# Performance work log

Measured on AMD Instinct MI355X. Metric: run time of the kernel, lower is better.

The kernel has to match this reference:

```python
import jax, jax.numpy as jnp
import numpy as np
import math

B, CK, T, H, W = 4, 64, 8, 30, 54
N, CV = 8, 512

def setup_inputs() -> dict:
    key = jax.random.key(0)
    k1, k2, k3, k4 = jax.random.split(key, 4)
    mem_keys = jax.random.normal(k1, (B, CK, T, H, W), dtype=jnp.float32)
    mem_values = jax.random.normal(k2, (N, CV, T, H, W), dtype=jnp.float32)
    qk = jax.random.normal(k3, (B, CK, H, W), dtype=jnp.float32)
    broadcast_map = jax.random.randint(k4, (N,), 0, B, dtype=jnp.int64)
    return {"mem_keys": mem_keys, "mem_values": mem_values, "qk": qk,
            "broadcast_map": broadcast_map}

def reference(mem_keys, mem_values, qk, broadcast_map):
    # STCNModel.read_memory
    Bq, CKq, Tq, Hq, Wq = mem_keys.shape
    mk = mem_keys.reshape(Bq, CKq, Tq * Hq * Wq)      # [B, CK, THW]
    q = qk.reshape(Bq, CKq, Hq * Wq)                   # [B, CK, HW]
    a_sq = jnp.sum(mk * mk, axis=1)[:, :, None]        # [B, THW, 1]
    ab = jnp.einsum('bct,bcq->btq', mk, q)             # [B, THW, HW]
    frame_affinity = (2.0 * ab - a_sq) / math.sqrt(CKq)
    # softmax over memory dim (axis=1)
    frame_affinity = jax.nn.softmax(frame_affinity, axis=1)
    obj_affinity = frame_affinity[broadcast_map]       # [N, THW, HW]
    Nn, CVv = mem_values.shape[0], mem_values.shape[1]
    mo = mem_values.reshape(Nn, CVv, Tq * Hq * Wq)     # [N, CV, THW]
    obj_read = jnp.einsum('nct,ntq->ncq', mo, obj_affinity)
    return obj_read.reshape(Nn, CVv, Hq, Wq)
```

## Files before the change

kernel.cpp:

```cpp
#include <hip/hip_runtime.h>
#include <hip/hip_bf16.h>

#define CKDIM 64
#define THW   12960
#define HWDIM 1620
#define NOBJ  8
#define CVAL  512
#define NB    4
#define NSTEP 405
#define NJT   13
#define NCHS  8
#define NCHP  4
#define PCH   16
#define S2F   0.3606737602222409f

#if defined(__has_builtin)
#if __has_builtin(__builtin_amdgcn_global_load_lds)
#define HAVE_GLL 1
#endif
#endif

using bf16x8 = __attribute__((ext_vector_type(8))) short;
using f32x4  = __attribute__((ext_vector_type(4))) float;

__device__ __forceinline__ unsigned cvtpk(float lo, float hi) {
    unsigned r;
    asm("v_cvt_pk_bf16_f32 %0, %1, %2" : "=v"(r) : "v"(lo), "v"(hi));
    return r;
}
__device__ __forceinline__ unsigned short bf_rne(float x) {
    unsigned u = __float_as_uint(x);
    u += 0x7FFFu + ((u >> 16) & 1u);
    return (unsigned short)(u >> 16);
}
__device__ __forceinline__ float fexp2(float x) {
#if __has_builtin(__builtin_amdgcn_exp2f)
    return __builtin_amdgcn_exp2f(x);
#else
    return __expf(x * 0.69314718055994531f);
#endif
}
#ifdef HAVE_GLL
__device__ __forceinline__ void gload16(const void* g, void* l) {
    __builtin_amdgcn_global_load_lds(
        (const __attribute__((address_space(1))) unsigned int*)g,
        (__attribute__((address_space(3))) unsigned int*)l, 16, 0, 0);
}
#endif

__global__ void stcn_ksq_kernel(const float* __restrict__ mk, float* __restrict__ k8l) {
    int t = blockIdx.x * 256 + threadIdx.x;
    if (t >= THW) return;
    int b = blockIdx.y;
    const float* p = mk + (size_t)b * CKDIM * THW + t;
    float s = 0.f;
#pragma unroll
    for (int c = 0; c < CKDIM; ++c) { float v = p[(size_t)c * THW]; s = fmaf(v, v, s); }
    k8l[b * THW + t] = s * (0.125f * 1.44269504088896341f);
}

__global__ __launch_bounds__(512)
void stcn_ktr_kernel(const float* __restrict__ mk, unsigned short* __restrict__ kbt,
                     float* __restrict__ k8l) {
    __shared__ unsigned short L[64][72];
    __shared__ float S[64][8];
    const int tid = threadIdx.x, b = blockIdx.y, t0 = blockIdx.x * 64;
    const int tt = tid & 63;
    float a2 = 0.f;
#pragma unroll
    for (int it = 0; it < 8; ++it) {
        int idx = tid + 512 * it;
        int c = idx >> 6;
        int t = t0 + tt;
        float v = (t < THW) ? mk[((size_t)b * CKDIM + c) * THW + t] : 0.f;
        L[tt][c] = bf_rne(v);
        a2 = fmaf(v, v, a2);
    }
    S[tt][tid >> 6] = a2;
    __syncthreads();
    if (tid < 64) {
        float s = 0.f;
#pragma unroll
        for (int q = 0; q < 8; ++q) s += S[tid][q];
        int t = t0 + tid;
        if (t < THW) k8l[b * THW + t] = s * (0.125f * 1.44269504088896341f);
    }
    {
        int tr = tid >> 3, cq = tid & 7;
        int t = t0 + tr;
        if (t < THW) {
            uint4 o = *(const uint4*)&L[tr][8 * cq];
            *(uint4*)(kbt + ((size_t)b * THW + t) * CKDIM + 8 * cq) = o;
        }
    }
}

__global__ void stcn_vcvt_kernel(const float* __restrict__ mv, unsigned short* __restrict__ mvb) {
    size_t i = ((size_t)blockIdx.x * 256 + threadIdx.x) * 8;
    if (i >= (size_t)NOBJ * CVAL * THW) return;
    float4 v0 = *(const float4*)(mv + i);
    float4 v1 = *(const float4*)(mv + i + 4);
    uint4 o;
    o.x = cvtpk(v0.x, v0.y); o.y = cvtpk(v0.z, v0.w);
    o.z = cvtpk(v1.x, v1.y); o.w = cvtpk(v1.z, v1.w);
    *(uint4*)(mvb + i) = o;
}

template <int MODE, bool VB16, bool KB16>
__global__ __launch_bounds__(512, (MODE == 1) ? 4 : 1)
void stcn_aff_kernel(const float* __restrict__ mk, const unsigned short* __restrict__ kbt,
                     const float* __restrict__ qk, const float* __restrict__ k8l,
                     float* __restrict__ mpart, float* __restrict__ lpart,
                     const float* __restrict__ mv, const unsigned short* __restrict__ mvb,
                     const int* __restrict__ bmap, float* __restrict__ out)
{
    constexpr int SMEM_BYTES = (MODE == 0) ? 36864 : 45312;
    __shared__ __align__(16) unsigned char smem[SMEM_BYTES];
    unsigned short* KtP   = (unsigned short*)smem;
    float*          k8tP  = (float*)(smem + 9216);
    unsigned short* PtP   = (unsigned short*)(smem + 9472);
    unsigned short* VtP   = (unsigned short*)(smem + 23808);
    float*          mjsP  = (float*)(smem + 44288);
    float*          iljsP = (float*)(smem + 44800);
    unsigned short* QtP   = (unsigned short*)smem;

    const int tid  = threadIdx.x;
    const int w    = tid >> 6;
    const int lane = tid & 63;
    const int g    = lane >> 4;
    const int lr   = lane & 15;

    int b, n = 0, jt, kc, cb = 0;
    if (MODE == 0) { b = blockIdx.y; jt = blockIdx.x >> 3; kc = blockIdx.x & 7; }
    else {
        n = blockIdx.y; jt = blockIdx.x >> 3; kc = (blockIdx.x >> 1) & 3; cb = blockIdx.x & 1;
        b = bmap[n];
    }
    const int jbase = jt * 128;
    const int cbase = cb * 256;

#pragma unroll
    for (int it = 0; it < 8; ++it) {
        int idx = tid + 512 * it;
        int j = idx & 127, cp = idx >> 7;
        int jg = jbase + j;
        float q0 = 0.f, q1 = 0.f;
        if (jg < HWDIM) {
            const float* qp = qk + ((size_t)b * CKDIM + 2 * cp) * HWDIM + jg;
            q0 = qp[0]; q1 = qp[HWDIM];
        }
        unsigned wh = cvtpk(q0, q1);
        float r0 = q0 - __uint_as_float(wh << 16);
        float r1 = q1 - __uint_as_float(wh & 0xFFFF0000u);
        *(unsigned*)&QtP[(0 * 128 + j) * 72 + 2 * cp] = wh;
        *(unsigned*)&QtP[(1 * 128 + j) * 72 + 2 * cp] = cvtpk(r0, r1);
    }
    __syncthreads();
    bf16x8 bqh[2], bql[2];
#pragma unroll
    for (int s = 0; s < 2; ++s) {
        bqh[s] = *(const bf16x8*)&QtP[(0 * 128 + w * 16 + lr) * 72 + 32 * s + 8 * g];
        bql[s] = *(const bf16x8*)&QtP[(1 * 128 + w * 16 + lr) * 72 + 32 * s + 8 * g];
    }
    __syncthreads();

    auto stageK_loads = [&](int st, uint2& k16, float2* kvf) {
        if constexpr (KB16) {
            int tt = tid >> 4, cq = tid & 15;
            k16 = *(const uint2*)(kbt + ((size_t)b * THW + st * 32 + tt) * CKDIM + 4 * cq);
        } else {
#pragma unroll
            for (int it = 0; it < 2; ++it) {
                int idx = tid + 512 * it;
                int tt = idx & 31, cp = idx >> 5;
                const float* kp = mk + ((size_t)b * CKDIM + 2 * cp) * THW + st * 32 + tt;
                kvf[it].x = kp[0];
                kvf[it].y = kp[THW];
            }
        }
    };
    auto stageK_write = [&](int buf, uint2 k16, const float2* kvf) {
        if constexpr (KB16) {
            int tt = tid >> 4, cq = tid & 15;
            *(uint2*)&KtP[(buf * 32 + tt) * 72 + 4 * cq] = k16;
        } else {
#pragma unroll
            for (int it = 0; it < 2; ++it) {
                int idx = tid + 512 * it;
                int tt = idx & 31, cp = idx >> 5;
                *(unsigned*)&KtP[(buf * 32 + tt) * 72 + 2 * cp] = cvtpk(kvf[it].x, kvf[it].y);
            }
        }
    };

    int s0, s1;
    if (MODE == 0) { s0 = (NSTEP * kc) / NCHS; s1 = (NSTEP * (kc + 1)) / NCHS; }
    else           { s0 = (NSTEP * kc) / NCHP; s1 = (NSTEP * (kc + 1)) / NCHP; }

    if (MODE == 1 && tid < 128) {
        int jg = jbase + tid;
        float m = 0.f, l = 0.f;
        if (jg < HWDIM) {
            m = -1e30f;
#pragma unroll
            for (int c = 0; c < NCHS; ++c) {
                float mc = mpart[(b * NCHS + c) * HWDIM + jg];
                float lc = lpart[(b * NCHS + c) * HWDIM + jg];
                float mn = fmaxf(m, mc);
                l = l * fexp2(m - mn) + lc * fexp2(mc - mn);
                m = mn;
            }
        }
        mjsP[tid]  = m;
        iljsP[tid] = (l > 0.f) ? 1.f / l : 0.f;
    }
    {
        uint2 k16; float2 kvf[2];
        stageK_loads(s0, k16, kvf);
        stageK_write(0, k16, kvf);
        if (tid < 32) k8tP[tid] = k8l[b * THW + s0 * 32 + tid];
    }
    __syncthreads();

    float mv_j = 0.f, il_j = 0.f;
    if (MODE == 1) { mv_j = mjsP[w * 16 + lr]; il_j = iljsP[w * 16 + lr]; }

    float m_run = -1e30f, l_run = 0.f;
    f32x4 zz = {0.f, 0.f, 0.f, 0.f};
    f32x4 acc[4][4];
    if (MODE == 1)
#pragma unroll
        for (int i = 0; i < 4; ++i)
#pragma unroll
            for (int j = 0; j < 4; ++j) acc[i][j] = zz;

    const int wc = w >> 1, wj = w & 1;
    const int vc = tid >> 1, vth = tid & 1;

    int cur = 0;
    for (int st = s0; st < s1; ++st) {
        const int t0 = st * 32;
        const bool nxt = (st + 1 < s1);

        uint4 vw0 = {0,0,0,0}, vw1 = {0,0,0,0};
        if (MODE == 1) {
            if (VB16) {
                const unsigned short* vp = mvb + ((size_t)n * CVAL + cbase + vc) * THW + t0 + vth * 16;
                vw0 = *(const uint4*)vp;
                vw1 = *(const uint4*)(vp + 8);
            } else {
                const float* vp = mv + ((size_t)n * CVAL + cbase + vc) * THW + t0 + vth * 16;
                float4 f0 = *(const float4*)vp;
                float4 f1 = *(const float4*)(vp + 4);
                float4 f2 = *(const float4*)(vp + 8);
                float4 f3 = *(const float4*)(vp + 12);
                vw0 = make_uint4(cvtpk(f0.x,f0.y), cvtpk(f0.z,f0.w), cvtpk(f1.x,f1.y), cvtpk(f1.z,f1.w));
                vw1 = make_uint4(cvtpk(f2.x,f2.y), cvtpk(f2.z,f2.w), cvtpk(f3.x,f3.y), cvtpk(f3.z,f3.w));
            }
        }
        uint2 k16; float2 kvf[2];
        float k8next = 0.f;
        if (nxt) {
            stageK_loads(st + 1, k16, kvf);
            if (tid < 32) k8next = k8l[b * THW + (st + 1) * 32 + tid];
        }
        bf16x8 ak0[2], ak1[2];
#pragma unroll
        for (int s = 0; s < 2; ++s) {
            ak0[s] = *(const bf16x8*)&KtP[(cur * 32 + lr) * 72 + 32 * s + 8 * g];
            ak1[s] = *(const bf16x8*)&KtP[(cur * 32 + 16 + lr) * 72 + 32 * s + 8 * g];
        }
        f32x4 k80 = *(const f32x4*)&k8tP[cur * 32 + 4 * g];
        f32x4 k81 = *(const f32x4*)&k8tP[cur * 32 + 16 + 4 * g];
        f32x4 ab0 = zz, ab1 = zz;
#pragma unroll
        for (int s = 0; s < 2; ++s) {
            ab0 = __builtin_amdgcn_mfma_f32_16x16x32_bf16(ak0[s], bqh[s], ab0, 0, 0, 0);
            ab0 = __builtin_amdgcn_mfma_f32_16x16x32_bf16(ak0[s], bql[s], ab0, 0, 0, 0);
            ab1 = __builtin_amdgcn_mfma_f32_16x16x32_bf16(ak1[s], bqh[s], ab1, 0, 0, 0);
            ab1 = __builtin_amdgcn_mfma_f32_16x16x32_bf16(ak1[s], bql[s], ab1, 0, 0, 0);
        }
        if (nxt) {
            stageK_write(cur ^ 1, k16, kvf);
            if (tid < 32) k8tP[(cur ^ 1) * 32 + tid] = k8next;
        }

        if (MODE == 0) {
            float L0[4], L1[4], tmax = -1e30f;
#pragma unroll
            for (int r = 0; r < 4; ++r) {
                L0[r] = fmaf(ab0[r], S2F, -k80[r]); tmax = fmaxf(tmax, L0[r]);
                L1[r] = fmaf(ab1[r], S2F, -k81[r]); tmax = fmaxf(tmax, L1[r]);
            }
            float ps = 0.f;
#pragma unroll
            for (int r = 0; r < 4; ++r)
                ps += fexp2(L0[r] - tmax) + fexp2(L1[r] - tmax);
            float mn = fmaxf(m_run, tmax);
            l_run = l_run * fexp2(m_run - mn) + ps * fexp2(tmax - mn);
            m_run = mn;
            __syncthreads();
        } else {
            float p0[4], p1[4];
#pragma unroll
            for (int r = 0; r < 4; ++r) {
                p0[r] = fexp2(fmaf(ab0[r], S2F, -k80[r]) - mv_j) * il_j;
                p1[r] = fexp2(fmaf(ab1[r], S2F, -k81[r]) - mv_j) * il_j;
            }
            __syncthreads();
            {
                int jl = w * 16 + lr;
                *(uint2*)&PtP[jl * 56 + 4 * g]      = make_uint2(cvtpk(p0[0], p0[1]), cvtpk(p0[2], p0[3]));
                *(uint2*)&PtP[jl * 56 + 16 + 4 * g] = make_uint2(cvtpk(p1[0], p1[1]), cvtpk(p1[2], p1[3]));
                *(uint4*)&VtP[vc * 40 + vth * 16]     = vw0;
                *(uint4*)&VtP[vc * 40 + vth * 16 + 8] = vw1;
            }
            __syncthreads();
            bf16x8 bp[4];
#pragma unroll
            for (int jf = 0; jf < 4; ++jf)
                bp[jf] = *(const bf16x8*)&PtP[(wj * 64 + jf * 16 + lr) * 56 + 8 * g];
#pragma unroll
            for (int cf = 0; cf < 4; ++cf) {
                bf16x8 av = *(const bf16x8*)&VtP[(wc * 64 + cf * 16 + lr) * 40 + 8 * g];
#pragma unroll
                for (int jf = 0; jf < 4; ++jf)
                    acc[cf][jf] = __builtin_amdgcn_mfma_f32_16x16x32_bf16(av, bp[jf], acc[cf][jf], 0, 0, 0);
            }
        }
        cur ^= 1;
    }

    if (MODE == 0) {
#pragma unroll
        for (int off = 16; off < 64; off <<= 1) {
            float mo = __shfl_xor(m_run, off, 64);
            float lo = __shfl_xor(l_run, off, 64);
            float mn = fmaxf(m_run, mo);
            l_run = l_run * fexp2(m_run - mn) + lo * fexp2(mo - mn);
            m_run = mn;
        }
        int jg = jbase + w * 16 + lr;
        if (g == 0 && jg < HWDIM) {
            mpart[(b * NCHS + kc) * HWDIM + jg] = m_run;
            lpart[(b * NCHS + kc) * HWDIM + jg] = l_run;
        }
    } else {
#pragma unroll
        for (int cf = 0; cf < 4; ++cf) {
#pragma unroll
            for (int jf = 0; jf < 4; ++jf) {
                int jg = jbase + wj * 64 + jf * 16 + lr;
                if (jg < HWDIM) {
                    int c = cbase + wc * 64 + cf * 16 + 4 * g;
                    float* op = out + ((size_t)n * CVAL + c) * HWDIM + jg;
#pragma unroll
                    for (int r = 0; r < 4; ++r)
                        atomicAdd(op + (size_t)r * HWDIM, acc[cf][jf][r]);
                }
            }
        }
    }
}

__global__ __launch_bounds__(512)
void stcn_pwrite_kernel(const unsigned short* __restrict__ kbt,
                        const float* __restrict__ qk, const float* __restrict__ k8l,
                        const float* __restrict__ mpart, const float* __restrict__ lpart,
                        unsigned short* __restrict__ Pws, int bbase)
{
    __shared__ __align__(16) unsigned char smem[36864];
    unsigned short* KtP   = (unsigned short*)smem;
    float*          k8tP  = (float*)(smem + 9216);
    unsigned short* PtP   = (unsigned short*)(smem + 9472);
    float*          mjsP  = (float*)(smem + 23808);
    float*          iljsP = (float*)(smem + 24320);
    unsigned short* QtP   = (unsigned short*)smem;

    const int tid  = threadIdx.x;
    const int w    = tid >> 6;
    const int lane = tid & 63;
    const int g    = lane >> 4;
    const int lr   = lane & 15;

    const int bb = blockIdx.y;
    const int b  = bbase + bb;
    const int jt = blockIdx.x >> 4, kc = blockIdx.x & 15;
    const int jbase = jt * 128;

#pragma unroll
    for (int it = 0; it < 8; ++it) {
        int idx = tid + 512 * it;
        int j = idx & 127, cp = idx >> 7;
        int jg = jbase + j;
        float q0 = 0.f, q1 = 0.f;
        if (jg < HWDIM) {
            const float* qp = qk + ((size_t)b * CKDIM + 2 * cp) * HWDIM + jg;
            q0 = qp[0]; q1 = qp[HWDIM];
        }
        unsigned wh = cvtpk(q0, q1);
        float r0 = q0 - __uint_as_float(wh << 16);
        float r1 = q1 - __uint_as_float(wh & 0xFFFF0000u);
        *(unsigned*)&QtP[(0 * 128 + j) * 72 + 2 * cp] = wh;
        *(unsigned*)&QtP[(1 * 128 + j) * 72 + 2 * cp] = cvtpk(r0, r1);
    }
    __syncthreads();
    bf16x8 bqh[2], bql[2];
#pragma unroll
    for (int s = 0; s < 2; ++s) {
        bqh[s] = *(const bf16x8*)&QtP[(0 * 128 + w * 16 + lr) * 72 + 32 * s + 8 * g];
        bql[s] = *(const bf16x8*)&QtP[(1 * 128 + w * 16 + lr) * 72 + 32 * s + 8 * g];
    }
    __syncthreads();

    const int s0 = (NSTEP * kc) / PCH, s1 = (NSTEP * (kc + 1)) / PCH;

    if (tid < 128) {
        int jg = jbase + tid;
        float m = 0.f, l = 0.f;
        if (jg < HWDIM) {
            m = -1e30f;
#pragma unroll
            for (int c = 0; c < NCHS; ++c) {
                float mc = mpart[(b * NCHS + c) * HWDIM + jg];
                float lc = lpart[(b * NCHS + c) * HWDIM + jg];
                float mn = fmaxf(m, mc);
                l = l * fexp2(m - mn) + lc * fexp2(mc - mn);
                m = mn;
            }
        }
        mjsP[tid]  = m;
        iljsP[tid] = (l > 0.f) ? 1.f / l : 0.f;
    }
    {
        int tt = tid >> 4, cq = tid & 15;
        uint2 k16 = *(const uint2*)(kbt + ((size_t)b * THW + s0 * 32 + tt) * CKDIM + 4 * cq);
        *(uint2*)&KtP[tt * 72 + 4 * cq] = k16;
        if (tid < 32) k8tP[tid] = k8l[b * THW + s0 * 32 + tid];
    }
    __syncthreads();

    const float mv_j = mjsP[w * 16 + lr], il_j = iljsP[w * 16 + lr];
    f32x4 zz = {0.f, 0.f, 0.f, 0.f};

    int cur = 0;
    for (int st = s0; st < s1; ++st) {
        const int t0 = st * 32;
        const bool nxt = (st + 1 < s1);
        uint2 k16;
        float k8next = 0.f;
        const int tt = tid >> 4, cq = tid & 15;
        if (nxt) {
            k16 = *(const uint2*)(kbt + ((size_t)b * THW + (st + 1) * 32 + tt) * CKDIM + 4 * cq);
            if (tid < 32) k8next = k8l[b * THW + (st + 1) * 32 + tid];
        }
        bf16x8 ak0[2], ak1[2];
#pragma unroll
        for (int s = 0; s < 2; ++s) {
            ak0[s] = *(const bf16x8*)&KtP[(cur * 32 + lr) * 72 + 32 * s + 8 * g];
            ak1[s] = *(const bf16x8*)&KtP[(cur * 32 + 16 + lr) * 72 + 32 * s + 8 * g];
        }
        f32x4 k80 = *(const f32x4*)&k8tP[cur * 32 + 4 * g];
        f32x4 k81 = *(const f32x4*)&k8tP[cur * 32 + 16 + 4 * g];
        f32x4 ab0 = zz, ab1 = zz;
#pragma unroll
        for (int s = 0; s < 2; ++s) {
            ab0 = __builtin_amdgcn_mfma_f32_16x16x32_bf16(ak0[s], bqh[s], ab0, 0, 0, 0);
            ab0 = __builtin_amdgcn_mfma_f32_16x16x32_bf16(ak0[s], bql[s], ab0, 0, 0, 0);
            ab1 = __builtin_amdgcn_mfma_f32_16x16x32_bf16(ak1[s], bqh[s], ab1, 0, 0, 0);
            ab1 = __builtin_amdgcn_mfma_f32_16x16x32_bf16(ak1[s], bql[s], ab1, 0, 0, 0);
        }
        if (nxt) {
            *(uint2*)&KtP[((cur ^ 1) * 32 + tt) * 72 + 4 * cq] = k16;
            if (tid < 32) k8tP[(cur ^ 1) * 32 + tid] = k8next;
        }
        float p0[4], p1[4];
#pragma unroll
        for (int r = 0; r < 4; ++r) {
            p0[r] = fexp2(fmaf(ab0[r], S2F, -k80[r]) - mv_j) * il_j;
            p1[r] = fexp2(fmaf(ab1[r], S2F, -k81[r]) - mv_j) * il_j;
        }
        __syncthreads();
        {
            int jl = w * 16 + lr;
            *(uint2*)&PtP[jl * 56 + 4 * g]      = make_uint2(cvtpk(p0[0], p0[1]), cvtpk(p0[2], p0[3]));
            *(uint2*)&PtP[jl * 56 + 16 + 4 * g] = make_uint2(cvtpk(p1[0], p1[1]), cvtpk(p1[2], p1[3]));
        }
        __syncthreads();
        {
            int jr = tid >> 2, qq = tid & 3;
            int jg = jbase + jr;
            if (jg < HWDIM)
                *(uint4*)(Pws + ((size_t)bb * HWDIM + jg) * THW + t0 + qq * 8) =
                    *(const uint4*)&PtP[jr * 56 + qq * 8];
        }
        cur ^= 1;
    }
}

template <bool FULLP>
__global__ __launch_bounds__(256, 4)
void stcn_gemm3_kernel(const unsigned short* __restrict__ mvb,
                       const unsigned short* __restrict__ Pws,
                       const int* __restrict__ bmap, float* __restrict__ out, int phase)
{
    __shared__ __align__(16) unsigned short Av[2][128 * 32];
    __shared__ __align__(16) unsigned short Bv[2][128 * 32];

    int n, cm, jn, ks, ksplit;
    if constexpr (FULLP) {
        int wg  = blockIdx.x;
        int vid = (wg & 7) * 208 + (wg >> 3);
        n = vid / 208;
        int r  = vid % 208;
        cm = r / 52;
        int r2 = r % 52;
        jn = r2 >> 2;
        ks = r2 & 3;
        ksplit = 4;
    } else {
        n = blockIdx.y;
        const int x = blockIdx.x;
        ks = x & 1;
        const int rest = x >> 1;
        jn = rest % NJT;
        cm = rest / NJT;
        ksplit = 2;
    }
    const int b = bmap[n];
    int bslot;
    if constexpr (FULLP) { bslot = b; }
    else { if ((b >> 1) != phase) return; bslot = b & 1; }

    const int jbase = jn * 128, cbase = cm * 128;

    const int tid = threadIdx.x;
    const int w = tid >> 6, lane = tid & 63, g = lane >> 4, lr = lane & 15;
    const int wc = w >> 1, wj = w & 1;

    const int srow = tid >> 2;
    const int tsw  = (((tid & 3) ^ ((tid >> 3) & 3)) << 3);
    const int gs8  = ((g ^ ((lr >> 1) & 3)) << 3);

    const int s0 = (NSTEP * ks) / ksplit, s1 = (NSTEP * (ks + 1)) / ksplit;

    const unsigned short* abase = mvb + ((size_t)n * CVAL + cbase) * THW;
    const unsigned short* bbase = Pws + (size_t)bslot * HWDIM * THW;
    int jr0 = jbase + srow;       if (jr0 >= HWDIM) jr0 = 0;
    int jr1 = jbase + 64 + srow;  if (jr1 >= HWDIM) jr1 = 0;
    const unsigned short* ga0 = abase + (size_t)(srow) * THW + tsw;
    const unsigned short* ga1 = abase + (size_t)(64 + srow) * THW + tsw;
    const unsigned short* gb0 = bbase + (size_t)jr0 * THW + tsw;
    const unsigned short* gb1 = bbase + (size_t)jr1 * THW + tsw;

    f32x4 zz = {0.f, 0.f, 0.f, 0.f};
    f32x4 acc[4][4];
#pragma unroll
    for (int i = 0; i < 4; ++i)
#pragma unroll
        for (int j = 0; j < 4; ++j) acc[i][j] = zz;

#ifdef HAVE_GLL
    auto stage = [&](int buf, int st) {
        const int t0 = st * 32;
        gload16(ga0 + t0, &Av[buf][0    + w * 512]);
        gload16(ga1 + t0, &Av[buf][2048 + w * 512]);
        gload16(gb0 + t0, &Bv[buf][0    + w * 512]);
        gload16(gb1 + t0, &Bv[buf][2048 + w * 512]);
    };
    stage(0, s0);
#else
    {
        const int t0 = s0 * 32;
        *(uint4*)&Av[0][tid * 8]        = *(const uint4*)(ga0 + t0);
        *(uint4*)&Av[0][2048 + tid * 8] = *(const uint4*)(ga1 + t0);
        *(uint4*)&Bv[0][tid * 8]        = *(const uint4*)(gb0 + t0);
        *(uint4*)&Bv[0][2048 + tid * 8] = *(const uint4*)(gb1 + t0);
    }
#endif
    __syncthreads();

    int cur = 0;
    for (int st = s0; st < s1; ++st) {
        const bool nxt = (st + 1 < s1);
#ifdef HAVE_GLL
        if (nxt) stage(cur ^ 1, st + 1);
#else
        uint4 ra0, ra1, rb0, rb1;
        if (nxt) {
            const int t0 = (st + 1) * 32;
            ra0 = *(const uint4*)(ga0 + t0);
            ra1 = *(const uint4*)(ga1 + t0);
            rb0 = *(const uint4*)(gb0 + t0);
            rb1 = *(const uint4*)(gb1 + t0);
        }
#endif
        bf16x8 av[4], bp[4];
#pragma unroll
        for (int cf = 0; cf < 4; ++cf)
            av[cf] = *(const bf16x8*)&Av[cur][(wc * 64 + cf * 16 + lr) * 32 + gs8];
#pragma unroll
        for (int jf = 0; jf < 4; ++jf)
            bp[jf] = *(const bf16x8*)&Bv[cur][(wj * 64 + jf * 16 + lr) * 32 + gs8];
#pragma unroll
        for (int cf = 0; cf < 4; ++cf)
#pragma unroll
            for (int jf = 0; jf < 4; ++jf)
                acc[cf][jf] = __builtin_amdgcn_mfma_f32_16x16x32_bf16(av[cf], bp[jf], acc[cf][jf], 0, 0, 0);
#ifndef HAVE_GLL
        if (nxt) {
            *(uint4*)&Av[cur ^ 1][tid * 8]        = ra0;
            *(uint4*)&Av[cur ^ 1][2048 + tid * 8] = ra1;
            *(uint4*)&Bv[cur ^ 1][tid * 8]        = rb0;
            *(uint4*)&Bv[cur ^ 1][2048 + tid * 8] = rb1;
        }
#endif
        __syncthreads();
        cur ^= 1;
    }

#pragma unroll
    for (int cf = 0; cf < 4; ++cf)
#pragma unroll
        for (int jf = 0; jf < 4; ++jf) {
            int jg = jbase + wj * 64 + jf * 16 + lr;
            if (jg < HWDIM) {
                int c = cbase + wc * 64 + cf * 16 + 4 * g;
                float* op = out + ((size_t)n * CVAL + c) * HWDIM + jg;
#pragma unroll
                for (int r = 0; r < 4; ++r)
                    atomicAdd(op + (size_t)r * HWDIM, acc[cf][jf][r]);
            }
        }
}

extern "C" void kernel_launch(void* const* d_in, const int* in_sizes, int n_in,
                              void* d_out, int out_size, void* d_ws, size_t ws_size,
                              hipStream_t stream) {
    (void)in_sizes; (void)n_in;
    const float* mk   = (const float*)d_in[0];
    const float* mv   = (const float*)d_in[1];
    const float* qkp  = (const float*)d_in[2];
    const int*   bmap = (const int*)d_in[3];
    float* out = (float*)d_out;

    float* k8l   = (float*)d_ws;
    float* mpart = k8l + NB * THW;
    float* lpart = mpart + NB * NCHS * HWDIM;
    unsigned short* mvb = (unsigned short*)(lpart + NB * NCHS * HWDIM);
    unsigned short* kbt = mvb + (size_t)NOBJ * CVAL * THW;
    unsigned short* Pws = kbt + (size_t)NB * THW * CKDIM;

    size_t base_bytes = (size_t)(NB * THW + 2 * NB * NCHS * HWDIM) * 4;
    size_t need_vb  = base_bytes + (size_t)NOBJ * CVAL * THW * 2;
    size_t need_kbt = need_vb + (size_t)NB * THW * CKDIM * 2;
    size_t need_P2  = need_kbt + (size_t)2 * HWDIM * THW * 2;
    size_t need_P4  = need_kbt + (size_t)4 * HWDIM * THW * 2;
    bool use_vb16 = (ws_size >= need_vb);
    bool use_kbt  = (ws_size >= need_kbt);
    bool use_P2   = (ws_size >= need_P2);
    bool use_P4   = (ws_size >= need_P4);

    hipMemsetAsync(d_out, 0, (size_t)out_size * sizeof(float), stream);
    if (use_kbt)
        stcn_ktr_kernel<<<dim3((THW + 63) / 64, NB), 512, 0, stream>>>(mk, kbt, k8l);
    else
        stcn_ksq_kernel<<<dim3((THW + 255) / 256, NB), 256, 0, stream>>>(mk, k8l);
    if (use_vb16) {
        size_t nthreads = (size_t)NOBJ * CVAL * THW / 8;
        stcn_vcvt_kernel<<<(unsigned)((nthreads + 255) / 256), 256, 0, stream>>>(mv, mvb);
    }

    if (use_kbt)
        stcn_aff_kernel<0, false, true><<<dim3(NJT * NCHS, NB), 512, 0, stream>>>(
            mk, kbt, qkp, k8l, mpart, lpart, nullptr, nullptr, nullptr, nullptr);
    else
        stcn_aff_kernel<0, false, false><<<dim3(NJT * NCHS, NB), 512, 0, stream>>>(
            mk, nullptr, qkp, k8l, mpart, lpart, nullptr, nullptr, nullptr, nullptr);

    if (use_P4 && use_kbt) {
        stcn_pwrite_kernel<<<dim3(NJT * PCH, NB), 512, 0, stream>>>(
            kbt, qkp, k8l, mpart, lpart, Pws, 0);
        stcn_gemm3_kernel<true><<<dim3(1664), 256, 0, stream>>>(
            mvb, Pws, bmap, out, 0);
    } else if (use_P2 && use_kbt) {
        for (int p = 0; p < 2; ++p) {
            stcn_pwrite_kernel<<<dim3(NJT * PCH, 2), 512, 0, stream>>>(
                kbt, qkp, k8l, mpart, lpart, Pws, 2 * p);
            stcn_gemm3_kernel<false><<<dim3(104, NOBJ), 256, 0, stream>>>(
                mvb, Pws, bmap, out, p);
        }
    } else {
        dim3 g1(NJT * NCHP * 2, NOBJ);
        if (use_vb16 && use_kbt)
            stcn_aff_kernel<1, true, true><<<g1, 512, 0, stream>>>(
                mk, kbt, qkp, k8l, mpart, lpart, nullptr, mvb, bmap, out);
        else if (use_vb16)
            stcn_aff_kernel<1, true, false><<<g1, 512, 0, stream>>>(
                mk, nullptr, qkp, k8l, mpart, lpart, nullptr, mvb, bmap, out);
        else
            stcn_aff_kernel<1, false, false><<<g1, 512, 0, stream>>>(
                mk, nullptr, qkp, k8l, mpart, lpart, mv, nullptr, bmap, out);
    }
}
```

Measured before the change: 526.0 us.

## Use 256x256 tiles with 1024-thread blocks for the value-affinity GEMM

Replaces the 128x128, 256-thread GEMM3 path with a new GEMM4 kernel for the full-P case. It uses 256x256 output tiles per workgroup across 16 waves, each wave still computing a 64x64 sub-tile, with a 4-way K split and 448 workgroups. Larger tiles halve the global/L2 traffic per MFMA for the A (values) and B (affinity) operands. The cost is fewer workgroups (448 versus 1664), more tile waste at the HW=1620 edge (1792 padded columns), heavier synchronisation across 16 waves, and 64 KB of LDS per block, which limits occupancy.

Result: slower. 557.6 us (+6.0%).

```diff
diff --git a/kernel.cpp b/kernel.cpp
--- a/kernel.cpp
+++ b/kernel.cpp
@@ -9,6 +9,7 @@
 #define NB    4
 #define NSTEP 405
 #define NJT   13
+#define NJT2  7
 #define NCHS  8
 #define NCHP  4
 #define PCH   16
@@ -498,7 +499,112 @@
     }
 }
 
-template <bool FULLP>
+__global__ __launch_bounds__(1024, 4)
+void stcn_gemm4_kernel(const unsigned short* __restrict__ mvb,
+                       const unsigned short* __restrict__ Pws,
+                       const int* __restrict__ bmap, float* __restrict__ out)
+{
+    __shared__ __align__(16) unsigned short Av[2][256 * 32];
+    __shared__ __align__(16) unsigned short Bv[2][256 * 32];
+
+    const int wg  = blockIdx.x;
+    const int vid = (wg & 7) * 56 + (wg >> 3);
+    const int n   = vid / 56;
+    const int r   = vid % 56;
+    const int cm  = r / 28;
+    const int r2  = r % 28;
+    const int ks  = r2 / 7;
+    const int jn  = r2 % 7;
+    const int b = bmap[n];
+    const int jbase = jn * 256, cbase = cm * 256;
+
+    const int tid = threadIdx.x;
+    const int w = tid >> 6, lane = tid & 63, g = lane >> 4, lr = lane & 15;
+    const int wc = w >> 2, wj = w & 3;
+
+    const int srow = tid >> 2;
+    const int tsw  = (((tid & 3) ^ ((tid >> 3) & 3)) << 3);
+    const int gs8  = ((g ^ ((lr >> 1) & 3)) << 3);
+
+    const int s0 = (NSTEP * ks) / 4, s1 = (NSTEP * (ks + 1)) / 4;
+
+    const unsigned short* ga = mvb + ((size_t)n * CVAL + cbase + srow) * THW + tsw;
+    int jr = jbase + srow; if (jr >= HWDIM) jr = 0;
+    const unsigned short* gb = Pws + ((size_t)b * HWDIM + jr) * THW + tsw;
+
+    f32x4 zz = {0.f, 0.f, 0.f, 0.f};
+    f32x4 acc[4][4];
+#pragma unroll
+    for (int i = 0; i < 4; ++i)
+#pragma unroll
+        for (int j = 0; j < 4; ++j) acc[i][j] = zz;
+
+#ifdef HAVE_GLL
+    auto stage = [&](int buf, int st) {
+        const int t0 = st * 32;
+        gload16(ga + t0, &Av[buf][w * 512]);
+        gload16(gb + t0, &Bv[buf][w * 512]);
+    };
+    stage(0, s0);
+#else
+    {
+        const int t0 = s0 * 32;
+        *(uint4*)&Av[0][tid * 8] = *(const uint4*)(ga + t0);
+        *(uint4*)&Bv[0][tid * 8] = *(const uint4*)(gb + t0);
+    }
+#endif
+    __syncthreads();
+
+    int cur = 0;
+    for (int st = s0; st < s1; ++st) {
+        const bool nxt = (st + 1 < s1);
+#ifdef HAVE_GLL
+        if (nxt) stage(cur ^ 1, st + 1);
+#else
+        uint4 ra, rb;
+        if (nxt) {
+            const int t0 = (st + 1) * 32;
+            ra = *(const uint4*)(ga + t0);
+            rb = *(const uint4*)(gb + t0);
+        }
+#endif
+        bf16x8 av[4], bp[4];
+#pragma unroll
+        for (int cf = 0; cf < 4; ++cf)
+            av[cf] = *(const bf16x8*)&Av[cur][(wc * 64 + cf * 16 + lr) * 32 + gs8];
+#pragma unroll
+        for (int jf = 0; jf < 4; ++jf)
+            bp[jf] = *(const bf16x8*)&Bv[cur][(wj * 64 + jf * 16 + lr) * 32 + gs8];
+#pragma unroll
+        for (int cf = 0; cf < 4; ++cf)
+#pragma unroll
+            for (int jf = 0; jf < 4; ++jf)
+                acc[cf][jf] = __builtin_amdgcn_mfma_f32_16x16x32_bf16(av[cf], bp[jf], acc[cf][jf], 0, 0, 0);
+#ifndef HAVE_GLL
+        if (nxt) {
+            *(uint4*)&Av[cur ^ 1][tid * 8] = ra;
+            *(uint4*)&Bv[cur ^ 1][tid * 8] = rb;
+        }
+#endif
+        __syncthreads();
+        cur ^= 1;
+    }
+
+#pragma unroll
+    for (int cf = 0; cf < 4; ++cf)
+#pragma unroll
+        for (int jf = 0; jf < 4; ++jf) {
+            int jg = jbase + wj * 64 + jf * 16 + lr;
+            if (jg < HWDIM) {
+                int c = cbase + wc * 64 + cf * 16 + 4 * g;
+                float* op = out + ((size_t)n * CVAL + c) * HWDIM + jg;
+#pragma unroll
+                for (int r4 = 0; r4 < 4; ++r4)
+                    atomicAdd(op + (size_t)r4 * HWDIM, acc[cf][jf][r4]);
+            }
+        }
+}
+
 __global__ __launch_bounds__(256, 4)
 void stcn_gemm3_kernel(const unsigned short* __restrict__ mvb,
                        const unsigned short* __restrict__ Pws,
@@ -507,31 +613,16 @@
     __shared__ __align__(16) unsigned short Av[2][128 * 32];
     __shared__ __align__(16) unsigned short Bv[2][128 * 32];
 
-    int n, cm, jn, ks, ksplit;
-    if constexpr (FULLP) {
-        int wg  = blockIdx.x;
-        int vid = (wg & 7) * 208 + (wg >> 3);
-        n = vid / 208;
-        int r  = vid % 208;
-        cm = r / 52;
-        int r2 = r % 52;
-        jn = r2 >> 2;
-        ks = r2 & 3;
-        ksplit = 4;
-    } else {
-        n = blockIdx.y;
-        const int x = blockIdx.x;
-        ks = x & 1;
-        const int rest = x >> 1;
-        jn = rest % NJT;
-        cm = rest / NJT;
-        ksplit = 2;
-    }
+    const int n = blockIdx.y;
     const int b = bmap[n];
-    int bslot;
-    if constexpr (FULLP) { bslot = b; }
-    else { if ((b >> 1) != phase) return; bslot = b & 1; }
-
+    if ((b >> 1) != phase) return;
+    const int bslot = b & 1;
+
+    const int x = blockIdx.x;
+    const int ks = x & 1;
+    const int rest = x >> 1;
+    const int jn = rest % NJT;
+    const int cm = rest / NJT;
     const int jbase = jn * 128, cbase = cm * 128;
 
     const int tid = threadIdx.x;
@@ -542,7 +633,7 @@
     const int tsw  = (((tid & 3) ^ ((tid >> 3) & 3)) << 3);
     const int gs8  = ((g ^ ((lr >> 1) & 3)) << 3);
 
-    const int s0 = (NSTEP * ks) / ksplit, s1 = (NSTEP * (ks + 1)) / ksplit;
+    const int s0 = (NSTEP * ks) / 2, s1 = (NSTEP * (ks + 1)) / 2;
 
     const unsigned short* abase = mvb + ((size_t)n * CVAL + cbase) * THW;
     const unsigned short* bbase = Pws + (size_t)bslot * HWDIM * THW;
@@ -628,8 +719,8 @@
                 int c = cbase + wc * 64 + cf * 16 + 4 * g;
                 float* op = out + ((size_t)n * CVAL + c) * HWDIM + jg;
 #pragma unroll
-                for (int r = 0; r < 4; ++r)
-                    atomicAdd(op + (size_t)r * HWDIM, acc[cf][jf][r]);
+                for (int r4 = 0; r4 < 4; ++r4)
+                    atomicAdd(op + (size_t)r4 * HWDIM, acc[cf][jf][r4]);
             }
         }
 }
@@ -681,13 +772,12 @@
     if (use_P4 && use_kbt) {
         stcn_pwrite_kernel<<<dim3(NJT * PCH, NB), 512, 0, stream>>>(
             kbt, qkp, k8l, mpart, lpart, Pws, 0);
-        stcn_gemm3_kernel<true><<<dim3(1664), 256, 0, stream>>>(
-            mvb, Pws, bmap, out, 0);
+        stcn_gemm4_kernel<<<dim3(448), 1024, 0, stream>>>(mvb, Pws, bmap, out);
     } else if (use_P2 && use_kbt) {
         for (int p = 0; p < 2; ++p) {
             stcn_pwrite_kernel<<<dim3(NJT * PCH, 2), 512, 0, stream>>>(
                 kbt, qkp, k8l, mpart, lpart, Pws, 2 * p);
-            stcn_gemm3_kernel<false><<<dim3(104, NOBJ), 256, 0, stream>>>(
+            stcn_gemm3_kernel<<<dim3(104, NOBJ), 256, 0, stream>>>(
                 mvb, Pws, bmap, out, p);
         }
     } else {
```
